# Performance work log

Hardware: AMD Instinct MI355X
Metric: run time of the kernel (lower is better)

The kernel has to match this reference:

```python
import jax, jax.numpy as jnp
import numpy as np

N = 500_000        # num nodes
E = 2_000_000      # num edges
D = 8              # message passing depth
DIM = 16           # dim_embed
F = 5              # NUM_NODE_FEATURES
NUM_DAGS = 5_000


def _mlp_params(key, d_in, d_out, scale=0.1):
    k1, k2, k3 = jax.random.split(key, 3)
    return (jax.random.normal(k1, (d_in, 16), jnp.float32) * scale, jnp.zeros((16,), jnp.float32),
            jax.random.normal(k2, (16, 8), jnp.float32) * scale, jnp.zeros((8,), jnp.float32),
            jax.random.normal(k3, (8, d_out), jnp.float32) * scale, jnp.zeros((d_out,), jnp.float32))


def _mlp(x, w1, b1, w2, b2, w3, b3):
    h = jax.nn.relu(x @ w1 + b1)
    h = jax.nn.relu(h @ w2 + b2)
    return h @ w3 + b3


def setup_inputs() -> dict:
    key = jax.random.key(0)
    ks = jax.random.split(key, 8)
    x = jax.random.normal(ks[0], (N, F), jnp.float32)
    edge_index = jax.random.randint(ks[1], (2, E), 0, N, jnp.int32)
    edge_mask_batch = jax.random.bernoulli(ks[2], 0.5, (D, E))
    ptr = jnp.arange(0, N + 1, N // NUM_DAGS, dtype=jnp.int32)  # 5000 dags of 100 nodes
    inp = {"x": x, "edge_index": edge_index, "edge_mask_batch": edge_mask_batch, "ptr": ptr}
    names = ["p", "m", "u", "d", "g"]
    dins = [F, DIM, DIM, F + DIM, DIM]
    for name, din, k in zip(names, dins, jax.random.split(ks[3], 5)):
        w1, b1, w2, b2, w3, b3 = _mlp_params(k, din, DIM)
        inp.update({f"{name}w1": w1, f"{name}b1": b1, f"{name}w2": w2,
                    f"{name}b2": b2, f"{name}w3": w3, f"{name}b3": b3})
    return inp


def reference(x, edge_index, edge_mask_batch, ptr,
              pw1, pb1, pw2, pb2, pw3, pb3,
              mw1, mb1, mw2, mb2, mw3, mb3,
              uw1, ub1, uw2, ub2, uw3, ub3,
              dw1, db1, dw2, db2, dw3, db3,
              gw1, gb1, gw2, gb2, gw3, gb3):
    num_nodes = x.shape[0]
    dst, src = edge_index[0], edge_index[1]

    # NodeEncoder: prep then D rounds of masked sparse message passing
    h = _mlp(x, pw1, pb1, pw2, pb2, pw3, pb3)  # [N, DIM]

    def step(h, mask):
        mf = mask.astype(h.dtype)  # [E]
        y = _mlp(h, mw1, mb1, mw2, mb2, mw3, mb3)  # [N, DIM]
        # adj @ y: out[i] = sum over active edges (i <- j) of y[j]
        agg = jnp.zeros_like(h).at[dst].add(y[src] * mf[:, None])
        # node_mask: nodes that are destinations of an active edge
        nm = (jnp.zeros((num_nodes,), h.dtype).at[dst].add(mf) > 0)
        upd = _mlp(agg, uw1, ub1, uw2, ub2, uw3, ub3)
        return h + nm[:, None].astype(h.dtype) * upd, None

    h, _ = jax.lax.scan(step, h, edge_mask_batch)
    node_embeddings = h

    # DagEncoder: per-dag segment-sum of mlp([x, h])
    num_dags = ptr.shape[0] - 1
    seg = jnp.searchsorted(ptr, jnp.arange(num_nodes, dtype=ptr.dtype), side='right') - 1
    z = _mlp(jnp.concatenate([x, node_embeddings], axis=1), dw1, db1, dw2, db2, dw3, db3)
    dag_summaries = jax.ops.segment_sum(z, seg, num_segments=num_dags)  # [num_dags, DIM]

    # GlobalEncoder: no obs_ptr -> sum over all dags
    g = _mlp(dag_summaries, gw1, gb1, gw2, gb2, gw3, gb3)
    global_summaries = g.sum(0)[None]  # [1, DIM]

    return node_embeddings, dag_summaries, global_summaries
```

## Files before the change

kernel.cpp:

```cpp
#include <hip/hip_runtime.h>
#include <hip/hip_bf16.h>
#include <stdint.h>

#define N_NODES 500000
#define N_EDGES 2000000
#define DEPTH 8
#define NUM_DAGS 5000
#define DAG_SZ 100
#define OUT_NODES_ELEMS 8000000
#define OUT_GLOB_OFF    8080000
#define NB_SCAN 489

typedef __hip_bfloat16 bf16;

__device__ __forceinline__ float bfb2f(unsigned u) {
    return __uint_as_float((u & 0xffffu) << 16);
}
__device__ __forceinline__ unsigned f2bfb(float f) {
    bf16 b = __float2bfloat16(f);
    unsigned short u;
    __builtin_memcpy(&u, &b, 2);
    return (unsigned)u;
}
__device__ __forceinline__ float rndbf(float f) { return bfb2f(f2bfb(f)); }
template<int ISBF>
__device__ __forceinline__ float crnd(float f) { return ISBF ? rndbf(f) : f; }

__device__ __forceinline__ void unpack_pair(uint4 a, uint4 b, float* f) {
    f[0]=bfb2f(a.x);  f[1]=bfb2f(a.x>>16);
    f[2]=bfb2f(a.y);  f[3]=bfb2f(a.y>>16);
    f[4]=bfb2f(a.z);  f[5]=bfb2f(a.z>>16);
    f[6]=bfb2f(a.w);  f[7]=bfb2f(a.w>>16);
    f[8]=bfb2f(b.x);  f[9]=bfb2f(b.x>>16);
    f[10]=bfb2f(b.y); f[11]=bfb2f(b.y>>16);
    f[12]=bfb2f(b.z); f[13]=bfb2f(b.z>>16);
    f[14]=bfb2f(b.w); f[15]=bfb2f(b.w>>16);
}
__device__ __forceinline__ unsigned packpair(float lo, float hi) {
    return f2bfb(lo) | (f2bfb(hi) << 16);
}
__device__ __forceinline__ void pack16(const float* f, uint4* a, uint4* b) {
    a->x = packpair(f[0],f[1]);   a->y = packpair(f[2],f[3]);
    a->z = packpair(f[4],f[5]);   a->w = packpair(f[6],f[7]);
    b->x = packpair(f[8],f[9]);   b->y = packpair(f[10],f[11]);
    b->z = packpair(f[12],f[13]); b->w = packpair(f[14],f[15]);
}

template<int ISBF>
__device__ __forceinline__ float ldf(const void* p, size_t i) {
    return ISBF ? __bfloat162float(((const bf16*)p)[i]) : ((const float*)p)[i];
}
template<int ISBF>
__device__ __forceinline__ void load16(const void* base, size_t row, float* f) {
    if (ISBF) {
        const uint4* p = (const uint4*)((const bf16*)base + row*16);
        uint4 a = p[0], b = p[1];
        unpack_pair(a, b, f);
    } else {
        const float4* p = (const float4*)((const float*)base + row*16);
        float4 v0=p[0], v1=p[1], v2=p[2], v3=p[3];
        f[0]=v0.x; f[1]=v0.y; f[2]=v0.z; f[3]=v0.w;
        f[4]=v1.x; f[5]=v1.y; f[6]=v1.z; f[7]=v1.w;
        f[8]=v2.x; f[9]=v2.y; f[10]=v2.z; f[11]=v2.w;
        f[12]=v3.x; f[13]=v3.y; f[14]=v3.z; f[15]=v3.w;
    }
}
template<int ISBF>
__device__ __forceinline__ void store16(void* base, size_t row, const float* f) {
    if (ISBF) {
        uint4 a, b; pack16(f, &a, &b);
        uint4* p = (uint4*)((bf16*)base + row*16);
        p[0] = a; p[1] = b;
    } else {
        float4* p = (float4*)((float*)base + row*16);
        p[0] = make_float4(f[0],f[1],f[2],f[3]);
        p[1] = make_float4(f[4],f[5],f[6],f[7]);
        p[2] = make_float4(f[8],f[9],f[10],f[11]);
        p[3] = make_float4(f[12],f[13],f[14],f[15]);
    }
}

__global__ void k_detect(const void* __restrict__ x, int* __restrict__ flag) {
    const unsigned short* u = (const unsigned short*)x;
    int t = threadIdx.x;
    int wild = 0;
    #pragma unroll
    for (int k = 0; k < 4; k++) {
        float v = bfb2f(u[t*4 + k]);
        if (fabsf(v) > 1000.f) wild = 1;
    }
    unsigned long long m = __ballot(wild);
    if (t == 0) flag[0] = (m == 0ull) ? 1 : 0;
}

template<int DIN, int ISBF>
__device__ __forceinline__ void load_mlp_smem(const void* w1, const void* b1,
        const void* w2, const void* b2, const void* w3, const void* b3,
        float* s) {
    const int n1 = DIN * 16;
    const int tot = n1 + 16 + 128 + 8 + 128 + 16;
    for (int i = threadIdx.x; i < tot; i += blockDim.x) {
        int o = i; float v;
        if (o < n1)                 v = ldf<ISBF>(w1, o);
        else if ((o -= n1) < 16)    v = ldf<ISBF>(b1, o);
        else if ((o -= 16) < 128)   v = ldf<ISBF>(w2, o);
        else if ((o -= 128) < 8)    v = ldf<ISBF>(b2, o);
        else if ((o -= 8) < 128)    v = ldf<ISBF>(w3, o);
        else                        v = ldf<ISBF>(b3, o - 128);
        s[i] = v;
    }
}

template<int DIN, int ISBF>
__device__ __forceinline__ void mlp_apply(const float* in, const float* s,
                                          float* out) {
    const float* w1 = s;
    const float* b1 = s + DIN * 16;
    const float* w2 = b1 + 16;
    const float* b2 = w2 + 128;
    const float* w3 = b2 + 8;
    const float* b3 = w3 + 128;
    float h1[16];
    #pragma unroll
    for (int j = 0; j < 16; j++) {
        float a = b1[j];
        #pragma unroll
        for (int i = 0; i < DIN; i++) a = fmaf(in[i], w1[i*16 + j], a);
        h1[j] = crnd<ISBF>(fmaxf(a, 0.f));
    }
    float h2[8];
    #pragma unroll
    for (int j = 0; j < 8; j++) {
        float a = b2[j];
        #pragma unroll
        for (int i = 0; i < 16; i++) a = fmaf(h1[i], w2[i*8 + j], a);
        h2[j] = crnd<ISBF>(fmaxf(a, 0.f));
    }
    #pragma unroll
    for (int j = 0; j < 16; j++) {
        float a = b3[j];
        #pragma unroll
        for (int i = 0; i < 8; i++) a = fmaf(h2[i], w3[i*16 + j], a);
        out[j] = crnd<ISBF>(a);
    }
}

__global__ __launch_bounds__(256)
void k_hist(const int* __restrict__ dstp, int* __restrict__ deg,
            unsigned short* __restrict__ rank) {
    int e = blockIdx.x * blockDim.x + threadIdx.x;
    if (e >= N_EDGES) return;
    rank[e] = (unsigned short)atomicAdd(&deg[dstp[e]], 1);
}

__global__ __launch_bounds__(256)
void k_bsum(const int* __restrict__ deg, int* __restrict__ bsum) {
    __shared__ int sd[256];
    int b = blockIdx.x, t = threadIdx.x;
    int base = b * 1024;
    int s = 0;
    #pragma unroll
    for (int k = 0; k < 4; k++) {
        int i = base + t + k * 256;
        if (i < N_NODES) s += deg[i];
    }
    sd[t] = s; __syncthreads();
    for (int off = 128; off > 0; off >>= 1) {
        if (t < off) sd[t] += sd[t + off];
        __syncthreads();
    }
    if (t == 0) bsum[b] = sd[0];
}

__global__ __launch_bounds__(512)
void k_bscan(const int* __restrict__ bsum, int* __restrict__ boff) {
    __shared__ int s[512];
    int t = threadIdx.x;
    int v = (t < NB_SCAN) ? bsum[t] : 0;
    s[t] = v; __syncthreads();
    for (int off = 1; off < 512; off <<= 1) {
        int x = (t >= off) ? s[t - off] : 0;
        __syncthreads();
        s[t] += x;
        __syncthreads();
    }
    if (t < NB_SCAN) boff[t] = s[t] - v;
}

__global__ __launch_bounds__(1024)
void k_scan(const int* __restrict__ deg, const int* __restrict__ boff,
            int* __restrict__ row_ptr) {
    __shared__ int s[1024];
    int b = blockIdx.x, t = threadIdx.x;
    int i = b * 1024 + t;
    int v = (i < N_NODES) ? deg[i] : 0;
    s[t] = v; __syncthreads();
    for (int off = 1; off < 1024; off <<= 1) {
        int x = (t >= off) ? s[t - off] : 0;
        __syncthreads();
        s[t] += x;
        __syncthreads();
    }
    int excl = boff[b] + s[t] - v;
    if (i < N_NODES) {
        row_ptr[i] = excl;
        if (i == N_NODES - 1) row_ptr[N_NODES] = excl + v;
    }
}

__global__ __launch_bounds__(256)
void k_scatter(const int* __restrict__ dstp, const int* __restrict__ srcp,
               const int* __restrict__ mask, const unsigned short* __restrict__ rank,
               const int* __restrict__ row_ptr, unsigned* __restrict__ csr) {
    int e = blockIdx.x * blockDim.x + threadIdx.x;
    if (e >= N_EDGES) return;
    unsigned mb = 0;
    #pragma unroll
    for (int t = 0; t < DEPTH; t++)
        mb |= (mask[(size_t)t * N_EDGES + e] != 0 ? 1u : 0u) << t;
    int d = dstp[e];
    int pos = row_ptr[d] + (int)rank[e];
    csr[pos] = (unsigned)srcp[e] | (mb << 19);
}


template<int ISBF>
__device__ __forceinline__ void prep_body(const void* x,
        const void* pw1, const void* pb1, const void* pw2,
        const void* pb2, const void* pw3, const void* pb3,
        const void* mw1, const void* mb1, const void* mw2,
        const void* mb2, const void* mw3, const void* mb3,
        void* h, bf16* y0, float* sp, float* sm) {
    load_mlp_smem<5, ISBF>(pw1, pb1, pw2, pb2, pw3, pb3, sp);
    load_mlp_smem<16, ISBF>(mw1, mb1, mw2, mb2, mw3, mb3, sm);
    __syncthreads();
    int i = blockIdx.x * blockDim.x + threadIdx.x;
    if (i >= N_NODES) return;
    float in[5];
    #pragma unroll
    for (int j = 0; j < 5; j++) in[j] = ldf<ISBF>(x, (size_t)i*5 + j);
    float hv[16];
    mlp_apply<5, ISBF>(in, sp, hv);
    store16<ISBF>(h, i, hv);
    float y[16];
    mlp_apply<16, ISBF>(hv, sm, y);
    uint4 oa, ob; pack16(y, &oa, &ob);
    uint4* yp = (uint4*)(y0 + (size_t)i*16);
    yp[0] = oa; yp[1] = ob;
}

__global__ __launch_bounds__(256, 4)
void k_prep(const void* __restrict__ x,
            const void* pw1, const void* pb1, const void* pw2,
            const void* pb2, const void* pw3, const void* pb3,
            const void* mw1, const void* mb1, const void* mw2,
            const void* mb2, const void* mw3, const void* mb3,
            void* __restrict__ h, bf16* __restrict__ y0,
            const int* __restrict__ dtflag) {
    __shared__ float sp[5*16 + 16 + 128 + 8 + 128 + 16];
    __shared__ float sm[16*16 + 16 + 128 + 8 + 128 + 16];
    if (dtflag[0])
        prep_body<1>(x, pw1,pb1,pw2,pb2,pw3,pb3, mw1,mb1,mw2,mb2,mw3,mb3, h, y0, sp, sm);
    else
        prep_body<0>(x, pw1,pb1,pw2,pb2,pw3,pb3, mw1,mb1,mw2,mb2,mw3,mb3, h, y0, sp, sm);
}

template<int ISBF>
__device__ __forceinline__ void round_body(void* h, const int* row_ptr,
        const unsigned* csr, const bf16* yin, bf16* yout,
        const void* uw1, const void* ub1, const void* uw2,
        const void* ub2, const void* uw3, const void* ub3,
        const void* mw1, const void* mb1, const void* mw2,
        const void* mb2, const void* mw3, const void* mb3,
        int t, float* su, float* sm) {
    load_mlp_smem<16, ISBF>(uw1, ub1, uw2, ub2, uw3, ub3, su);
    load_mlp_smem<16, ISBF>(mw1, mb1, mw2, mb2, mw3, mb3, sm);
    __syncthreads();
    int i = blockIdx.x * blockDim.x + threadIdx.x;
    if (i >= N_NODES) return;
    int beg = row_ptr[i], end = row_ptr[i + 1];
    float acc[16];
    #pragma unroll
    for (int j = 0; j < 16; j++) acc[j] = 0.f;
    int any = 0;
    const unsigned tb = 1u << (19 + t);
    for (int p = beg; p < end; p += 6) {
        unsigned v[6];
        #pragma unroll
        for (int k = 0; k < 6; k++)
            v[k] = (p + k < end) ? __builtin_nontemporal_load(csr + p + k) : 0u;
        uint4 ga[6], gb[6];
        int act[6];
        #pragma unroll
        for (int k = 0; k < 6; k++) {
            act[k] = (v[k] & tb) != 0;
            if (act[k]) {
                int s = v[k] & 0x7FFFF;
                const uint4* yp = (const uint4*)(yin + (size_t)s*16);
                ga[k] = yp[0]; gb[k] = yp[1];
            }
        }
        #pragma unroll
        for (int k = 0; k < 6; k++) {
            if (act[k]) {
                any = 1;
                float f[16]; unpack_pair(ga[k], gb[k], f);
                #pragma unroll
                for (int j = 0; j < 16; j++) acc[j] += f[j];
            }
        }
    }
    uint4* yo = (uint4*)(yout + (size_t)i*16);
    if (!any) {
        const uint4* yp = (const uint4*)(yin + (size_t)i*16);
        yo[0] = yp[0]; yo[1] = yp[1];
        return;
    }
    #pragma unroll
    for (int j = 0; j < 16; j++) acc[j] = crnd<ISBF>(acc[j]);
    float upd[16];
    mlp_apply<16, ISBF>(acc, su, upd);
    float hv[16];
    load16<ISBF>(h, i, hv);
    float o[16];
    #pragma unroll
    for (int j = 0; j < 16; j++) o[j] = crnd<ISBF>(hv[j] + upd[j]);
    store16<ISBF>(h, i, o);
    float yn[16];
    mlp_apply<16, ISBF>(o, sm, yn);
    uint4 oa, ob; pack16(yn, &oa, &ob);
    yo[0] = oa; yo[1] = ob;
}

__global__ __launch_bounds__(256, 6)
void k_round(void* __restrict__ h, const int* __restrict__ row_ptr,
             const unsigned* __restrict__ csr,
             const bf16* __restrict__ yin, bf16* __restrict__ yout,
             const void* uw1, const void* ub1, const void* uw2,
             const void* ub2, const void* uw3, const void* ub3,
             const void* mw1, const void* mb1, const void* mw2,
             const void* mb2, const void* mw3, const void* mb3,
             int t, const int* __restrict__ dtflag) {
    __shared__ float su[16*16 + 16 + 128 + 8 + 128 + 16];
    __shared__ float sm[16*16 + 16 + 128 + 8 + 128 + 16];
    if (dtflag[0])
        round_body<1>(h, row_ptr, csr, yin, yout, uw1,ub1,uw2,ub2,uw3,ub3,
                      mw1,mb1,mw2,mb2,mw3,mb3, t, su, sm);
    else
        round_body<0>(h, row_ptr, csr, yin, yout, uw1,ub1,uw2,ub2,uw3,ub3,
                      mw1,mb1,mw2,mb2,mw3,mb3, t, su, sm);
}

template<int ISBF>
__device__ __forceinline__ void dag_body(const void* x, const void* h,
        const void* w1, const void* b1, const void* w2,
        const void* b2, const void* w3, const void* b3,
        float* dagsum, float* s, float* zb) {
    load_mlp_smem<21, ISBF>(w1, b1, w2, b2, w3, b3, s);
    __syncthreads();
    int t = threadIdx.x;
    int dag = blockIdx.x;
    if (t < DAG_SZ) {
        int i = dag * DAG_SZ + t;
        float in[21];
        #pragma unroll
        for (int j = 0; j < 5; j++) in[j] = ldf<ISBF>(x, (size_t)i*5 + j);
        load16<ISBF>(h, i, in + 5);
        float z[16];
        mlp_apply<21, ISBF>(in, s, z);
        #pragma unroll
        for (int j = 0; j < 16; j++) zb[t*16 + j] = z[j];
    }
    __syncthreads();
    if (t < 16) {
        float acc = 0.f;
        for (int r = 0; r < DAG_SZ; r++) acc += zb[r*16 + t];
        dagsum[(size_t)dag*16 + t] = acc;
    }
}

__global__ __launch_bounds__(128)
void k_dag(const void* __restrict__ x, const void* __restrict__ h,
           const void* w1, const void* b1, const void* w2,
           const void* b2, const void* w3, const void* b3,
           float* __restrict__ dagsum, const int* __restrict__ dtflag) {
    __shared__ float s[21*16 + 16 + 128 + 8 + 128 + 16];
    __shared__ float zb[DAG_SZ * 16];
    if (dtflag[0]) dag_body<1>(x, h, w1,b1,w2,b2,w3,b3, dagsum, s, zb);
    else           dag_body<0>(x, h, w1,b1,w2,b2,w3,b3, dagsum, s, zb);
}

template<int ISBF>
__device__ __forceinline__ void glob_body(const float* dagsum,
        const void* w1, const void* b1, const void* w2,
        const void* b2, const void* w3, const void* b3,
        void* d_out, float* globacc, float* s, float* gb) {
    load_mlp_smem<16, ISBF>(w1, b1, w2, b2, w3, b3, s);
    __syncthreads();
    int t = threadIdx.x;
    int d = blockIdx.x * blockDim.x + t;
    float g[16];
    if (d < NUM_DAGS) {
        const float4* dp = (const float4*)(dagsum + (size_t)d*16);
        float4 v0 = dp[0], v1 = dp[1], v2 = dp[2], v3 = dp[3];
        float in[16] = { v0.x, v0.y, v0.z, v0.w, v1.x, v1.y, v1.z, v1.w,
                         v2.x, v2.y, v2.z, v2.w, v3.x, v3.y, v3.z, v3.w };
        #pragma unroll
        for (int j = 0; j < 16; j++) in[j] = crnd<ISBF>(in[j]);
        if (ISBF) {
            bf16* od = (bf16*)d_out + OUT_NODES_ELEMS;
            store16<1>(od, d, in);
        } else {
            float* od = (float*)d_out + OUT_NODES_ELEMS;
            store16<0>(od, d, in);
        }
        mlp_apply<16, ISBF>(in, s, g);
    } else {
        #pragma unroll
        for (int j = 0; j < 16; j++) g[j] = 0.f;
    }
    #pragma unroll
    for (int j = 0; j < 16; j++) gb[t*16 + j] = g[j];
    __syncthreads();
    if (t < 16) {
        float acc = 0.f;
        for (int r = 0; r < 256; r++) acc += gb[r*16 + t];
        unsafeAtomicAdd(&globacc[t], acc);
    }
}

__global__ __launch_bounds__(256)
void k_glob(const float* __restrict__ dagsum,
            const void* w1, const void* b1, const void* w2,
            const void* b2, const void* w3, const void* b3,
            void* __restrict__ d_out, float* __restrict__ globacc,
            const int* __restrict__ dtflag) {
    __shared__ float s[16*16 + 16 + 128 + 8 + 128 + 16];
    __shared__ float gb[256 * 16];
    if (dtflag[0]) glob_body<1>(dagsum, w1,b1,w2,b2,w3,b3, d_out, globacc, s, gb);
    else           glob_body<0>(dagsum, w1,b1,w2,b2,w3,b3, d_out, globacc, s, gb);
}

__global__ void k_final(const float* __restrict__ globacc,
                        void* __restrict__ d_out, const int* __restrict__ dtflag) {
    const int isbf = dtflag[0];
    int t = threadIdx.x;
    if (t < 16) {
        if (isbf) ((bf16*)d_out)[OUT_GLOB_OFF + t] = __float2bfloat16(globacc[t]);
        else      ((float*)d_out)[OUT_GLOB_OFF + t] = globacc[t];
    }
}

extern "C" void kernel_launch(void* const* d_in, const int* in_sizes, int n_in,
                              void* d_out, int out_size, void* d_ws, size_t ws_size,
                              hipStream_t stream) {
    const void* x    = d_in[0];
    const int*  ei   = (const int*)d_in[1];
    const int*  mask = (const int*)d_in[2];
    const void* W[30];
    for (int i = 0; i < 30; i++) W[i] = d_in[4 + i];

    const int* dstp = ei;
    const int* srcp = ei + N_EDGES;

    char*           ws      = (char*)d_ws;
    int*            deg     = (int*)           (ws);
    float*          globacc = (float*)         (ws + 2000000);
    int*            dtflag  = (int*)           (ws + 2000064);
    int*            row_ptr = (int*)           (ws + 2000128);
    int*            bsum    = (int*)           (ws + 4000192);
    int*            boff    = (int*)           (ws + 4002240);
    unsigned*       csr     = (unsigned*)      (ws + 4004288);
    bf16*           y0      = (bf16*)          (ws + 12004288);
    bf16*           y1      = (bf16*)          (ws + 28004288);
    float*          dagsum  = (float*)         (ws + 44004288);
    unsigned short* rank    = (unsigned short*)(ws + 44324288);

    hipMemsetAsync(d_ws, 0, 2000064, stream);

    const int TB  = 256;
    const int nbN = (N_NODES + TB - 1) / TB;
    const int nbE = (N_EDGES + TB - 1) / TB;

    k_detect<<<1, 64, 0, stream>>>(x, dtflag);

    k_hist<<<nbE, TB, 0, stream>>>(dstp, deg, rank);
    k_bsum<<<NB_SCAN, 256, 0, stream>>>(deg, bsum);
    k_bscan<<<1, 512, 0, stream>>>(bsum, boff);
    k_scan<<<NB_SCAN, 1024, 0, stream>>>(deg, boff, row_ptr);
    k_scatter<<<nbE, TB, 0, stream>>>(dstp, srcp, mask, rank, row_ptr, csr);

    k_prep<<<nbN, TB, 0, stream>>>(x, W[0], W[1], W[2], W[3], W[4], W[5],
                                   W[6], W[7], W[8], W[9], W[10], W[11],
                                   d_out, y0, dtflag);
    bf16* yb[2] = { y0, y1 };
    for (int t = 0; t < DEPTH; t++) {
        k_round<<<nbN, TB, 0, stream>>>(d_out, row_ptr, csr,
                                        yb[t & 1], yb[(t + 1) & 1],
                                        W[12], W[13], W[14], W[15], W[16], W[17],
                                        W[6], W[7], W[8], W[9], W[10], W[11],
                                        t, dtflag);
    }
    k_dag<<<NUM_DAGS, 128, 0, stream>>>(x, d_out, W[18], W[19], W[20], W[21],
                                        W[22], W[23], dagsum, dtflag);
    k_glob<<<(NUM_DAGS + TB - 1) / TB, TB, 0, stream>>>(dagsum, W[24], W[25], W[26],
                                                        W[27], W[28], W[29],
                                                        d_out, globacc, dtflag);
    k_final<<<1, 64, 0, stream>>>(globacc, d_out, dtflag);
}
```

Baseline: 802.6 us.

## Build CSR via two-level bucketed counting sort instead of global atomics

```diff
diff --git a/kernel.cpp b/kernel.cpp
--- a/kernel.cpp
+++ b/kernel.cpp
@@ -9,7 +9,13 @@
 #define DAG_SZ 100
 #define OUT_NODES_ELEMS 8000000
 #define OUT_GLOB_OFF    8080000
-#define NB_SCAN 489
+
+#define EPB 1024
+#define NB_E 1954
+#define NBUK 256
+#define NBUK_USED 245
+#define MHIST (NBUK * NB_E)
+#define NB_SCAN2 489
 
 typedef __hip_bfloat16 bf16;
 
@@ -145,16 +151,24 @@
     }
 }
 
+
 __global__ __launch_bounds__(256)
-void k_hist(const int* __restrict__ dstp, int* __restrict__ deg,
-            unsigned short* __restrict__ rank) {
-    int e = blockIdx.x * blockDim.x + threadIdx.x;
-    if (e >= N_EDGES) return;
-    rank[e] = (unsigned short)atomicAdd(&deg[dstp[e]], 1);
+void k_bhist(const int* __restrict__ dstp, int* __restrict__ bh) {
+    __shared__ int hcnt[NBUK];
+    int t = threadIdx.x, blk = blockIdx.x;
+    hcnt[t] = 0;
+    __syncthreads();
+    #pragma unroll
+    for (int k = 0; k < 4; k++) {
+        int e = blk * EPB + k * 256 + t;
+        if (e < N_EDGES) atomicAdd(&hcnt[dstp[e] >> 11], 1);
+    }
+    __syncthreads();
+    bh[t * NB_E + blk] = hcnt[t];
 }
 
 __global__ __launch_bounds__(256)
-void k_bsum(const int* __restrict__ deg, int* __restrict__ bsum) {
+void k_gbsum(const int* __restrict__ v, int n, int* __restrict__ bsum) {
     __shared__ int sd[256];
     int b = blockIdx.x, t = threadIdx.x;
     int base = b * 1024;
@@ -162,7 +176,7 @@
     #pragma unroll
     for (int k = 0; k < 4; k++) {
         int i = base + t + k * 256;
-        if (i < N_NODES) s += deg[i];
+        if (i < n) s += v[i];
     }
     sd[t] = s; __syncthreads();
     for (int off = 128; off > 0; off >>= 1) {
@@ -173,10 +187,10 @@
 }
 
 __global__ __launch_bounds__(512)
-void k_bscan(const int* __restrict__ bsum, int* __restrict__ boff) {
+void k_gbscan(const int* __restrict__ bsum, int nb, int* __restrict__ boff) {
     __shared__ int s[512];
     int t = threadIdx.x;
-    int v = (t < NB_SCAN) ? bsum[t] : 0;
+    int v = (t < nb) ? bsum[t] : 0;
     s[t] = v; __syncthreads();
     for (int off = 1; off < 512; off <<= 1) {
         int x = (t >= off) ? s[t - off] : 0;
@@ -184,43 +198,92 @@
         s[t] += x;
         __syncthreads();
     }
-    if (t < NB_SCAN) boff[t] = s[t] - v;
+    if (t < nb) boff[t] = s[t] - v;
 }
 
 __global__ __launch_bounds__(1024)
-void k_scan(const int* __restrict__ deg, const int* __restrict__ boff,
-            int* __restrict__ row_ptr) {
+void k_gscan(const int* __restrict__ v, const int* __restrict__ boff, int n,
+             int* __restrict__ out) {
     __shared__ int s[1024];
     int b = blockIdx.x, t = threadIdx.x;
     int i = b * 1024 + t;
-    int v = (i < N_NODES) ? deg[i] : 0;
-    s[t] = v; __syncthreads();
+    int x = (i < n) ? v[i] : 0;
+    s[t] = x; __syncthreads();
     for (int off = 1; off < 1024; off <<= 1) {
-        int x = (t >= off) ? s[t - off] : 0;
-        __syncthreads();
-        s[t] += x;
-        __syncthreads();
-    }
-    int excl = boff[b] + s[t] - v;
-    if (i < N_NODES) {
-        row_ptr[i] = excl;
-        if (i == N_NODES - 1) row_ptr[N_NODES] = excl + v;
-    }
+        int y = (t >= off) ? s[t - off] : 0;
+        __syncthreads();
+        s[t] += y;
+        __syncthreads();
+    }
+    if (i < n) out[i] = boff[b] + s[t] - x;
 }
 
 __global__ __launch_bounds__(256)
-void k_scatter(const int* __restrict__ dstp, const int* __restrict__ srcp,
-               const int* __restrict__ mask, const unsigned short* __restrict__ rank,
-               const int* __restrict__ row_ptr, unsigned* __restrict__ csr) {
-    int e = blockIdx.x * blockDim.x + threadIdx.x;
-    if (e >= N_EDGES) return;
-    unsigned mb = 0;
-    #pragma unroll
-    for (int t = 0; t < DEPTH; t++)
-        mb |= (mask[(size_t)t * N_EDGES + e] != 0 ? 1u : 0u) << t;
-    int d = dstp[e];
-    int pos = row_ptr[d] + (int)rank[e];
-    csr[pos] = (unsigned)srcp[e] | (mb << 19);
+void k_bscatter(const int* __restrict__ dstp, const int* __restrict__ srcp,
+                const int* __restrict__ mask, const int* __restrict__ sbh,
+                uint2* __restrict__ staging) {
+    __shared__ int cur[NBUK];
+    int t = threadIdx.x, blk = blockIdx.x;
+    cur[t] = sbh[t * NB_E + blk];
+    __syncthreads();
+    #pragma unroll
+    for (int k = 0; k < 4; k++) {
+        int e = blk * EPB + k * 256 + t;
+        if (e < N_EDGES) {
+            int d = dstp[e];
+            unsigned mb = 0;
+            #pragma unroll
+            for (int tt = 0; tt < DEPTH; tt++)
+                mb |= (__builtin_nontemporal_load(mask + (size_t)tt * N_EDGES + e)
+                       != 0 ? 1u : 0u) << tt;
+            int pos = atomicAdd(&cur[d >> 11], 1);
+            staging[pos] = make_uint2((unsigned)srcp[e] | (mb << 19), (unsigned)d);
+        }
+    }
+}
+
+__global__ __launch_bounds__(256)
+void k_place(const uint2* __restrict__ staging, const int* __restrict__ sbh,
+             int* __restrict__ row_ptr, unsigned* __restrict__ csr) {
+    __shared__ int cnt[2048];
+    __shared__ int tsum[256];
+    int t = threadIdx.x, b = blockIdx.x;
+    int ebase = sbh[b * NB_E];
+    int eend  = sbh[(b + 1) * NB_E];
+    int nrec  = eend - ebase;
+    #pragma unroll
+    for (int k = 0; k < 8; k++) cnt[t + k * 256] = 0;
+    __syncthreads();
+    for (int r = t; r < nrec; r += 256)
+        atomicAdd(&cnt[staging[ebase + r].y & 2047], 1);
+    __syncthreads();
+    int s = 0;
+    #pragma unroll
+    for (int j = 0; j < 8; j++) { int c = cnt[t*8 + j]; cnt[t*8 + j] = s; s += c; }
+    int own = s;
+    tsum[t] = s;
+    __syncthreads();
+    for (int off = 1; off < 256; off <<= 1) {
+        int v = (t >= off) ? tsum[t - off] : 0;
+        __syncthreads();
+        tsum[t] += v;
+        __syncthreads();
+    }
+    int pref = tsum[t] - own + ebase;
+    #pragma unroll
+    for (int j = 0; j < 8; j++) cnt[t*8 + j] += pref;
+    int base_node = b * 2048;
+    #pragma unroll
+    for (int j = 0; j < 8; j++) {
+        int idx = base_node + t*8 + j;
+        if (idx <= N_NODES) row_ptr[idx] = cnt[t*8 + j];
+    }
+    __syncthreads();
+    for (int r = t; r < nrec; r += 256) {
+        uint2 u = staging[ebase + r];
+        int pos = atomicAdd(&cnt[u.y & 2047], 1);
+        csr[pos] = u.x;
+    }
 }
 
 
@@ -332,7 +395,7 @@
     yo[0] = oa; yo[1] = ob;
 }
 
-__global__ __launch_bounds__(256, 6)
+__global__ __launch_bounds__(256, 4)
 void k_round(void* __restrict__ h, const int* __restrict__ row_ptr,
              const unsigned* __restrict__ csr,
              const bf16* __restrict__ yin, bf16* __restrict__ yout,
@@ -463,32 +526,33 @@
     const int* dstp = ei;
     const int* srcp = ei + N_EDGES;
 
-    char*           ws      = (char*)d_ws;
-    int*            deg     = (int*)           (ws);
-    float*          globacc = (float*)         (ws + 2000000);
-    int*            dtflag  = (int*)           (ws + 2000064);
-    int*            row_ptr = (int*)           (ws + 2000128);
-    int*            bsum    = (int*)           (ws + 4000192);
-    int*            boff    = (int*)           (ws + 4002240);
-    unsigned*       csr     = (unsigned*)      (ws + 4004288);
-    bf16*           y0      = (bf16*)          (ws + 12004288);
-    bf16*           y1      = (bf16*)          (ws + 28004288);
-    float*          dagsum  = (float*)         (ws + 44004288);
-    unsigned short* rank    = (unsigned short*)(ws + 44324288);
-
-    hipMemsetAsync(d_ws, 0, 2000064, stream);
+    char*     ws      = (char*)d_ws;
+    float*    globacc = (float*)   (ws);
+    int*      dtflag  = (int*)     (ws + 64);
+    int*      row_ptr = (int*)     (ws + 128);
+    int*      bh      = (int*)     (ws + 2000192);
+    int*      sbh     = (int*)     (ws + 4001152);
+    int*      bsum    = (int*)     (ws + 6002176);
+    int*      boff    = (int*)     (ws + 6004224);
+    unsigned* csr     = (unsigned*)(ws + 6006272);
+    bf16*     y0      = (bf16*)    (ws + 14006272);
+    bf16*     y1      = (bf16*)    (ws + 30006272);
+    uint2*    staging = (uint2*)   (ws + 30006272);
+    float*    dagsum  = (float*)   (ws + 46006272);
+
+    hipMemsetAsync(d_ws, 0, 128, stream);
 
     const int TB  = 256;
     const int nbN = (N_NODES + TB - 1) / TB;
-    const int nbE = (N_EDGES + TB - 1) / TB;
 
     k_detect<<<1, 64, 0, stream>>>(x, dtflag);
 
-    k_hist<<<nbE, TB, 0, stream>>>(dstp, deg, rank);
-    k_bsum<<<NB_SCAN, 256, 0, stream>>>(deg, bsum);
-    k_bscan<<<1, 512, 0, stream>>>(bsum, boff);
-    k_scan<<<NB_SCAN, 1024, 0, stream>>>(deg, boff, row_ptr);
-    k_scatter<<<nbE, TB, 0, stream>>>(dstp, srcp, mask, rank, row_ptr, csr);
+    k_bhist<<<NB_E, 256, 0, stream>>>(dstp, bh);
+    k_gbsum<<<NB_SCAN2, 256, 0, stream>>>(bh, MHIST, bsum);
+    k_gbscan<<<1, 512, 0, stream>>>(bsum, NB_SCAN2, boff);
+    k_gscan<<<NB_SCAN2, 1024, 0, stream>>>(bh, boff, MHIST, sbh);
+    k_bscatter<<<NB_E, 256, 0, stream>>>(dstp, srcp, mask, sbh, staging);
+    k_place<<<NBUK_USED, 256, 0, stream>>>(staging, sbh, row_ptr, csr);
 
     k_prep<<<nbN, TB, 0, stream>>>(x, W[0], W[1], W[2], W[3], W[4], W[5],
                                    W[6], W[7], W[8], W[9], W[10], W[11],
```

New measurement: 679.0 us. 15.4% less time.
